# Kernel tuning notes

Measured on AMD Instinct MI355X. Metric: run time of the kernel, lower is better.

## Reference

```python
import jax, jax.numpy as jnp
import numpy as np

B, T, C, N = 4, 2048, 1024, 16
D = C // N


def setup_inputs() -> dict:
    key = jax.random.key(0)
    ks = jax.random.split(key, 10)
    s = 1.0 / np.sqrt(C)
    x = jax.random.normal(ks[0], (B, T, C), dtype=jnp.float32)
    token_mask = jax.random.randint(ks[1], (B, T), 0, 2, dtype=jnp.int32)
    token_mask = token_mask.at[:, 0].set(1)  # keep col 0 valid so no all--inf row
    inp = {"x": x, "token_mask": token_mask}
    for i, name in enumerate(["q", "k", "v", "p"]):
        inp[f"w{name}"] = jax.random.uniform(ks[2 + 2 * i], (C, C), jnp.float32, -s, s)
        inp[f"b{name}"] = jax.random.uniform(ks[3 + 2 * i], (C,), jnp.float32, -s, s)
    return inp


def reference(x, token_mask, wq, bq, wk, bk, wv, bv, wp, bp):
    # projections: nn.Linear computes x @ W.T + b
    q = (x @ wq.T + bq).reshape(B, T, N, D)
    k = (x @ wk.T + bk).reshape(B, T, N, D)
    v = (x @ wv.T + bv).reshape(B, T, N, D)
    # scores: (B, N, T, T)
    scores = jnp.einsum("bqnd,bknd->bnqk", q, k) / jnp.sqrt(jnp.float32(D))
    causal = jnp.tril(jnp.ones((T, T), dtype=bool))
    valid = causal[None, None] & (token_mask[:, None, None, :] != 0)
    scores = jnp.where(valid, scores, -jnp.inf)
    probs = jax.nn.softmax(scores, axis=-1)
    attn = jnp.einsum("bnqk,bknd->bqnd", probs, v).reshape(B, T, C)
    out = attn @ wp.T + bp
    return out
```

## Files before the change

kernel.cpp:

```cpp
#include <hip/hip_runtime.h>
#include <hip/hip_bf16.h>
#include <math.h>

typedef short bf16x8 __attribute__((ext_vector_type(8)));
typedef float f32x4 __attribute__((ext_vector_type(4)));

#if __has_builtin(__builtin_amdgcn_exp2f)
#define EXP2F(x) __builtin_amdgcn_exp2f(x)
#else
#define EXP2F(x) __expf(0.69314718056f * (x))
#endif

__device__ __forceinline__ unsigned short f2bf(float f) {
    union { float f; unsigned u; } v; v.f = f;
    unsigned r = v.u + 0x7fffu + ((v.u >> 16) & 1u);
    return (unsigned short)(r >> 16);
}

__device__ __forceinline__ unsigned pack_bf2(float a, float b) {
    __hip_bfloat162 h = __float22bfloat162_rn(float2{a, b});
    union { __hip_bfloat162 h; unsigned u; } c; c.h = h;
    return c.u;
}

__device__ __forceinline__ void gld_lds16(const unsigned short* g, const unsigned short* l) {
    __builtin_amdgcn_global_load_lds(
        (const __attribute__((address_space(1))) void*)g,
        (__attribute__((address_space(3))) void*)l, 16, 0, 0);
}

__global__ void cvt_f32_bf16(const float* __restrict__ src, unsigned short* __restrict__ dst, int n) {
    int i = (blockIdx.x * blockDim.x + threadIdx.x) * 4;
    if (i < n) {
        float4 f = *(const float4*)(src + i);
        ushort4 o;
        o.x = f2bf(f.x); o.y = f2bf(f.y); o.z = f2bf(f.z); o.w = f2bf(f.w);
        *(ushort4*)(dst + i) = o;
    }
}

__global__ void cvt4_f32_bf16(const float* s0, const float* s1, const float* s2, const float* s3,
                              unsigned short* d0, unsigned short* d1, unsigned short* d2,
                              unsigned short* d3, int n) {
    const float* s; unsigned short* d;
    switch (blockIdx.y) {
        case 0: s = s0; d = d0; break;
        case 1: s = s1; d = d1; break;
        case 2: s = s2; d = d2; break;
        default: s = s3; d = d3; break;
    }
    int i = (blockIdx.x * blockDim.x + threadIdx.x) * 4;
    if (i < n) {
        float4 f = *(const float4*)(s + i);
        ushort4 o;
        o.x = f2bf(f.x); o.y = f2bf(f.y); o.z = f2bf(f.z); o.w = f2bf(f.w);
        *(ushort4*)(d + i) = o;
    }
}

__global__ void mask_to_f(const int* __restrict__ tm, float* __restrict__ ma, int n) {
    int i = blockIdx.x * blockDim.x + threadIdx.x;
    if (i < n) ma[i] = tm[i] ? -24.0f : -__builtin_inff();
}

__global__ __launch_bounds__(256, 4) void gemm_bt(
        const unsigned short* __restrict__ A, const unsigned short* __restrict__ W,
        const float* __restrict__ b0p, const float* __restrict__ b1p,
        const float* __restrict__ b2p, float* __restrict__ outF,
        unsigned short* __restrict__ outB, unsigned short* __restrict__ vt,
        int M, int Nlog, int K) {
    __shared__ __align__(16) unsigned short As[2][128][32];
    __shared__ __align__(16) unsigned short Ws[2][128][32];
    const size_t BUFS = (size_t)8192 * 1024;
    const int m0 = blockIdx.y * 128, n0 = blockIdx.x * 128;
    const int tid = threadIdx.x, lane = tid & 63, w = tid >> 6;
    const int quad = lane >> 4, lc = lane & 15;
    const int wr = (w >> 1) * 64, wc = (w & 1) * 64;
    const int sr = lane >> 2;
    const int sc = (((lane & 3) ^ ((lane >> 3) & 3))) * 8;
    const int rp = (quad ^ ((lc >> 1) & 3)) * 8;

    const int buf = n0 >> 10;
    const float* bias = buf == 0 ? b0p : (buf == 1 ? b1p : b2p);

    auto stage = [&](int s, int k0) {
        gld_lds16(A + (size_t)(m0 + w * 32 +      sr) * K + k0 + sc, &As[s][w * 32     ][0]);
        gld_lds16(A + (size_t)(m0 + w * 32 + 16 + sr) * K + k0 + sc, &As[s][w * 32 + 16][0]);
        gld_lds16(W + (size_t)(n0 + w * 32 +      sr) * K + k0 + sc, &Ws[s][w * 32     ][0]);
        gld_lds16(W + (size_t)(n0 + w * 32 + 16 + sr) * K + k0 + sc, &Ws[s][w * 32 + 16][0]);
    };

    f32x4 acc[4][4] = {};
    stage(0, 0);

    for (int k0 = 0; k0 < K; k0 += 32) {
        const int cur = (k0 >> 5) & 1;
        __syncthreads();
        if (k0 + 32 < K) stage(cur ^ 1, k0 + 32);
        bf16x8 af[4], bw[4];
        #pragma unroll
        for (int i = 0; i < 4; ++i) af[i] = *(const bf16x8*)&As[cur][wr + i * 16 + lc][rp];
        #pragma unroll
        for (int j = 0; j < 4; ++j) bw[j] = *(const bf16x8*)&Ws[cur][wc + j * 16 + lc][rp];
        #pragma unroll
        for (int i = 0; i < 4; ++i)
            #pragma unroll
            for (int j = 0; j < 4; ++j)
                acc[i][j] = __builtin_amdgcn_mfma_f32_16x16x32_bf16(af[i], bw[j], acc[i][j], 0, 0, 0);
    }

    #pragma unroll
    for (int j = 0; j < 4; ++j) {
        int col = n0 + wc + j * 16 + lc;
        int coll = col & 1023;
        float bj = bias[coll];
        #pragma unroll
        for (int i = 0; i < 4; ++i) {
            int rowb = m0 + wr + i * 16 + quad * 4;
            if (buf == 2) {
                int bb = rowb >> 11, t = rowb & 2047;
                int hh = coll >> 6, dd = coll & 63;
                ushort4 o4;
                o4.x = f2bf(acc[i][j][0] + bj);
                o4.y = f2bf(acc[i][j][1] + bj);
                o4.z = f2bf(acc[i][j][2] + bj);
                o4.w = f2bf(acc[i][j][3] + bj);
                *(ushort4*)(vt + ((size_t)(bb * 16 + hh) * 64 + dd) * 2048 + t) = o4;
            } else {
                #pragma unroll
                for (int r = 0; r < 4; ++r) {
                    float v = acc[i][j][r] + bj;
                    size_t idx = (size_t)buf * BUFS + (size_t)(rowb + r) * 1024 + coll;
                    if (outB) outB[idx] = f2bf(v);
                    else      outF[idx] = v;
                }
            }
        }
    }
}

__global__ __launch_bounds__(256, 4) void attn_kernel(
        const unsigned short* __restrict__ Q, const unsigned short* __restrict__ K,
        const unsigned short* __restrict__ Vt, const float* __restrict__ maskadd,
        unsigned short* __restrict__ O) {
    const int T = 2048, C = 1024;
    __shared__ __align__(16) unsigned short Kl[64][64];
    __shared__ __align__(16) unsigned short Vl[2][64][64];
    __shared__ __align__(16) unsigned short Pl[4][16][72];

    const int pair = blockIdx.x;
    const int bn = blockIdx.y;
    const int b = bn >> 4, h = bn & 15;
    const int tid = threadIdx.x, w = tid >> 6, lane = tid & 63;
    const int quad = lane >> 4, lc = lane & 15;
    const float NEG_INF = -__builtin_inff();
    const float CSC = 0.18033688011112042f;

    const unsigned short* Kbh = K + (size_t)b * T * C + h * 64;
    const unsigned short* Vbh = Vt + (size_t)(b * 16 + h) * 64 * 2048;

    const int lrow = lane >> 3;
    const int swz8 = ((lane & 7) ^ (lrow & 7)) * 8;
    const int kb0 = (quad ^ (lc & 7)) * 8;

    auto stageK = [&](int kt) {
        #pragma unroll
        for (int ch = 0; ch < 2; ++ch)
            gld_lds16(Kbh + (size_t)(kt * 64 + w * 16 + ch * 8 + lrow) * C + swz8,
                      &Kl[w * 16 + ch * 8][0]);
    };
    auto stageV = [&](int kt, int s) {
        #pragma unroll
        for (int ch = 0; ch < 2; ++ch)
            gld_lds16(Vbh + (size_t)(w * 16 + ch * 8 + lrow) * 2048 + kt * 64 + swz8,
                      &Vl[s][w * 16 + ch * 8][0]);
    };

    #pragma unroll 1
    for (int half = 0; half < 2; ++half) {
        const int qt = half ? (31 - pair) : pair;

        if (half) __syncthreads();
        stageK(0);
        stageV(0, 0);

        size_t qrow = (size_t)(b * T + qt * 64 + w * 16 + lc) * C + h * 64;
        bf16x8 qb0 = *(const bf16x8*)(Q + qrow + quad * 8);
        bf16x8 qb1 = *(const bf16x8*)(Q + qrow + 32 + quad * 8);

        f32x4 oaccT[4] = {};
        float lsum = 0.f;
        const int qg = qt * 64 + w * 16 + lc;

        #pragma unroll 1
        for (int kt = 0; kt <= qt; ++kt) {
            const int slot = kt & 1;
            __syncthreads();

            f32x4 mk[4];
            #pragma unroll
            for (int j = 0; j < 4; ++j)
                mk[j] = *(const f32x4*)(maskadd + b * T + kt * 64 + j * 16 + quad * 4);

            f32x4 sacc[4] = {};
            #pragma unroll
            for (int j = 0; j < 4; ++j) {
                bf16x8 ka0 = *(const bf16x8*)&Kl[j * 16 + lc][kb0];
                bf16x8 ka1 = *(const bf16x8*)&Kl[j * 16 + lc][kb0 ^ 32];
                sacc[j] = __builtin_amdgcn_mfma_f32_16x16x32_bf16(ka0, qb0, sacc[j], 0, 0, 0);
                sacc[j] = __builtin_amdgcn_mfma_f32_16x16x32_bf16(ka1, qb1, sacc[j], 0, 0, 0);
            }

            __syncthreads();
            if (kt < qt) {
                stageK(kt + 1);
                stageV(kt + 1, slot ^ 1);
            }

            float p[4][4];
            #pragma unroll
            for (int j = 0; j < 4; ++j) {
                #pragma unroll
                for (int r = 0; r < 4; ++r) {
                    float sv = fmaf(sacc[j][r], CSC, mk[j][r]);
                    if (kt == qt) {
                        int kg = kt * 64 + j * 16 + quad * 4 + r;
                        if (kg > qg) sv = NEG_INF;
                    }
                    float pv = EXP2F(sv);
                    p[j][r] = pv;
                    lsum += pv;
                }
            }

            #pragma unroll
            for (int j = 0; j < 4; ++j) {
                uint2 pk;
                pk.x = pack_bf2(p[j][0], p[j][1]);
                pk.y = pack_bf2(p[j][2], p[j][3]);
                *(uint2*)&Pl[w][lc][j * 16 + quad * 4] = pk;
            }
            bf16x8 pb0 = *(const bf16x8*)&Pl[w][lc][quad * 8];
            bf16x8 pb1 = *(const bf16x8*)&Pl[w][lc][32 + quad * 8];

            #pragma unroll
            for (int jd = 0; jd < 4; ++jd) {
                bf16x8 va0 = *(const bf16x8*)&Vl[slot][jd * 16 + lc][kb0];
                bf16x8 va1 = *(const bf16x8*)&Vl[slot][jd * 16 + lc][kb0 ^ 32];
                oaccT[jd] = __builtin_amdgcn_mfma_f32_16x16x32_bf16(va0, pb0, oaccT[jd], 0, 0, 0);
                oaccT[jd] = __builtin_amdgcn_mfma_f32_16x16x32_bf16(va1, pb1, oaccT[jd], 0, 0, 0);
            }
        }

        lsum += __shfl_xor(lsum, 16, 64);
        lsum += __shfl_xor(lsum, 32, 64);
        float inv = 1.0f / lsum;
        size_t orow = (size_t)(b * T + qt * 64 + w * 16 + lc) * C + h * 64;
        #pragma unroll
        for (int jd = 0; jd < 4; ++jd) {
            ushort4 o4;
            o4.x = f2bf(oaccT[jd][0] * inv);
            o4.y = f2bf(oaccT[jd][1] * inv);
            o4.z = f2bf(oaccT[jd][2] * inv);
            o4.w = f2bf(oaccT[jd][3] * inv);
            *(ushort4*)(O + orow + jd * 16 + quad * 4) = o4;
        }
    }
}

extern "C" void kernel_launch(void* const* d_in, const int* in_sizes, int n_in,
                              void* d_out, int out_size, void* d_ws, size_t ws_size,
                              hipStream_t stream) {
    const float* x  = (const float*)d_in[0];
    const int* tm   = (const int*)d_in[1];
    const float* wq = (const float*)d_in[2]; const float* bq = (const float*)d_in[3];
    const float* wk = (const float*)d_in[4]; const float* bk = (const float*)d_in[5];
    const float* wv = (const float*)d_in[6]; const float* bv = (const float*)d_in[7];
    const float* wp = (const float*)d_in[8]; const float* bp = (const float*)d_in[9];
    float* out = (float*)d_out;

    const int Bv = 4, Tv = 2048, Cv = 1024;
    const size_t MT = (size_t)Bv * Tv;
    const size_t XN = MT * Cv;
    const size_t WN = (size_t)Cv * Cv;

    unsigned short* xb  = (unsigned short*)d_ws;
    unsigned short* wqb = xb  + XN;
    unsigned short* wkb = wqb + WN;
    unsigned short* wvb = wkb + WN;
    unsigned short* wpb = wvb + WN;
    unsigned short* Qb  = wpb + WN;
    unsigned short* Kb  = Qb + XN;
    unsigned short* Vtb = Kb + XN;
    unsigned short* Ab  = xb;
    float* maskadd = (float*)d_out;

    cvt_f32_bf16<<<XN / 1024, 256, 0, stream>>>(x, xb, (int)XN);
    cvt4_f32_bf16<<<dim3(WN / 1024, 4), 256, 0, stream>>>(wq, wk, wv, wp, wqb, wkb, wvb, wpb, (int)WN);
    mask_to_f<<<(int)(MT / 256), 256, 0, stream>>>(tm, maskadd, (int)MT);

    gemm_bt<<<dim3(24, 64), 256, 0, stream>>>(xb, wqb, bq, bk, bv, nullptr, Qb, Vtb, (int)MT, 3072, Cv);

    attn_kernel<<<dim3(16, Bv * 16), 256, 0, stream>>>(Qb, Kb, Vtb, maskadd, Ab);

    gemm_bt<<<dim3(8, 64), 256, 0, stream>>>(Ab, wpb, bp, bp, bp, out, nullptr, nullptr, (int)MT, 1024, Cv);
}
```

Before: 305.5 us.

## Widen attention blocks to 128 query rows and load GEMM W fragments directly

The attention kernel now uses 512-thread blocks covering 128 query rows, so each K/V tile staged in LDS is shared by eight waves instead of four. K and V staging is split across the two wave groups, and blocks are remapped on a flattened grid so each XCD handles a contiguous set of heads. The causal mask test moves into a separate diagonal-tile branch. Separately, the projection GEMM drops the LDS staging of W and has each lane read its W fragments straight from global memory, which lowers LDS use but adds uncoalesced global loads on every K step.

```diff
diff --git a/kernel.cpp b/kernel.cpp
--- a/kernel.cpp
+++ b/kernel.cpp
@@ -70,7 +70,6 @@
         unsigned short* __restrict__ outB, unsigned short* __restrict__ vt,
         int M, int Nlog, int K) {
     __shared__ __align__(16) unsigned short As[2][128][32];
-    __shared__ __align__(16) unsigned short Ws[2][128][32];
     const size_t BUFS = (size_t)8192 * 1024;
     const int m0 = blockIdx.y * 128, n0 = blockIdx.x * 128;
     const int tid = threadIdx.x, lane = tid & 63, w = tid >> 6;
@@ -83,25 +82,31 @@
     const int buf = n0 >> 10;
     const float* bias = buf == 0 ? b0p : (buf == 1 ? b1p : b2p);
 
-    auto stage = [&](int s, int k0) {
+    auto stageA = [&](int s, int k0) {
         gld_lds16(A + (size_t)(m0 + w * 32 +      sr) * K + k0 + sc, &As[s][w * 32     ][0]);
         gld_lds16(A + (size_t)(m0 + w * 32 + 16 + sr) * K + k0 + sc, &As[s][w * 32 + 16][0]);
-        gld_lds16(W + (size_t)(n0 + w * 32 +      sr) * K + k0 + sc, &Ws[s][w * 32     ][0]);
-        gld_lds16(W + (size_t)(n0 + w * 32 + 16 + sr) * K + k0 + sc, &Ws[s][w * 32 + 16][0]);
     };
 
+    const unsigned short* wp0 = W + (size_t)(n0 + wc +  0 + lc) * K + quad * 8;
+    const unsigned short* wp1 = W + (size_t)(n0 + wc + 16 + lc) * K + quad * 8;
+    const unsigned short* wp2 = W + (size_t)(n0 + wc + 32 + lc) * K + quad * 8;
+    const unsigned short* wp3 = W + (size_t)(n0 + wc + 48 + lc) * K + quad * 8;
+
     f32x4 acc[4][4] = {};
-    stage(0, 0);
+    stageA(0, 0);
 
     for (int k0 = 0; k0 < K; k0 += 32) {
         const int cur = (k0 >> 5) & 1;
         __syncthreads();
-        if (k0 + 32 < K) stage(cur ^ 1, k0 + 32);
-        bf16x8 af[4], bw[4];
+        if (k0 + 32 < K) stageA(cur ^ 1, k0 + 32);
+        bf16x8 bw[4];
+        bw[0] = *(const bf16x8*)(wp0 + k0);
+        bw[1] = *(const bf16x8*)(wp1 + k0);
+        bw[2] = *(const bf16x8*)(wp2 + k0);
+        bw[3] = *(const bf16x8*)(wp3 + k0);
+        bf16x8 af[4];
         #pragma unroll
         for (int i = 0; i < 4; ++i) af[i] = *(const bf16x8*)&As[cur][wr + i * 16 + lc][rp];
-        #pragma unroll
-        for (int j = 0; j < 4; ++j) bw[j] = *(const bf16x8*)&Ws[cur][wc + j * 16 + lc][rp];
         #pragma unroll
         for (int i = 0; i < 4; ++i)
             #pragma unroll
@@ -139,20 +144,23 @@
     }
 }
 
-__global__ __launch_bounds__(256, 4) void attn_kernel(
+__global__ __launch_bounds__(512, 4) void attn_kernel(
         const unsigned short* __restrict__ Q, const unsigned short* __restrict__ K,
         const unsigned short* __restrict__ Vt, const float* __restrict__ maskadd,
         unsigned short* __restrict__ O) {
     const int T = 2048, C = 1024;
     __shared__ __align__(16) unsigned short Kl[64][64];
     __shared__ __align__(16) unsigned short Vl[2][64][64];
-    __shared__ __align__(16) unsigned short Pl[4][16][72];
-
-    const int pair = blockIdx.x;
-    const int bn = blockIdx.y;
+    __shared__ __align__(16) unsigned short Pl[8][16][72];
+
+    const int bi = blockIdx.x;
+    const int xcd = bi & 7, rr = bi >> 3;
+    const int bn = xcd * 8 + (rr & 7);
+    const int pair = rr >> 3;
     const int b = bn >> 4, h = bn & 15;
     const int tid = threadIdx.x, w = tid >> 6, lane = tid & 63;
     const int quad = lane >> 4, lc = lane & 15;
+    const int wsub = w & 3, qhalf = w >> 2;
     const float NEG_INF = -__builtin_inff();
     const float CSC = 0.18033688011112042f;
 
@@ -163,38 +171,41 @@
     const int swz8 = ((lane & 7) ^ (lrow & 7)) * 8;
     const int kb0 = (quad ^ (lc & 7)) * 8;
 
-    auto stageK = [&](int kt) {
-        #pragma unroll
-        for (int ch = 0; ch < 2; ++ch)
-            gld_lds16(Kbh + (size_t)(kt * 64 + w * 16 + ch * 8 + lrow) * C + swz8,
-                      &Kl[w * 16 + ch * 8][0]);
+    auto stageKV = [&](int kt, int s) {
+        if (w < 4) {
+            #pragma unroll
+            for (int ch = 0; ch < 2; ++ch)
+                gld_lds16(Kbh + (size_t)(kt * 64 + w * 16 + ch * 8 + lrow) * C + swz8,
+                          &Kl[w * 16 + ch * 8][0]);
+        } else {
+            int wv = w - 4;
+            #pragma unroll
+            for (int ch = 0; ch < 2; ++ch)
+                gld_lds16(Vbh + (size_t)(wv * 16 + ch * 8 + lrow) * 2048 + kt * 64 + swz8,
+                          &Vl[s][wv * 16 + ch * 8][0]);
+        }
     };
-    auto stageV = [&](int kt, int s) {
-        #pragma unroll
-        for (int ch = 0; ch < 2; ++ch)
-            gld_lds16(Vbh + (size_t)(w * 16 + ch * 8 + lrow) * 2048 + kt * 64 + swz8,
-                      &Vl[s][w * 16 + ch * 8][0]);
-    };
 
     #pragma unroll 1
-    for (int half = 0; half < 2; ++half) {
-        const int qt = half ? (31 - pair) : pair;
-
-        if (half) __syncthreads();
-        stageK(0);
-        stageV(0, 0);
-
-        size_t qrow = (size_t)(b * T + qt * 64 + w * 16 + lc) * C + h * 64;
+    for (int hf = 0; hf < 2; ++hf) {
+        const int qt = hf ? (15 - pair) : pair;
+        const int kmax = 2 * qt + 1;
+
+        if (hf) __syncthreads();
+        stageKV(0, 0);
+
+        size_t qrow = (size_t)(b * T + qt * 128 + qhalf * 64 + wsub * 16 + lc) * C + h * 64;
         bf16x8 qb0 = *(const bf16x8*)(Q + qrow + quad * 8);
         bf16x8 qb1 = *(const bf16x8*)(Q + qrow + 32 + quad * 8);
 
         f32x4 oaccT[4] = {};
         float lsum = 0.f;
-        const int qg = qt * 64 + w * 16 + lc;
+        const int qg = qt * 128 + qhalf * 64 + wsub * 16 + lc;
 
         #pragma unroll 1
-        for (int kt = 0; kt <= qt; ++kt) {
+        for (int kt = 0; kt <= kmax; ++kt) {
             const int slot = kt & 1;
+            const bool dtile = (kt >= 2 * qt);
             __syncthreads();
 
             f32x4 mk[4];
@@ -212,25 +223,30 @@
             }
 
             __syncthreads();
-            if (kt < qt) {
-                stageK(kt + 1);
-                stageV(kt + 1, slot ^ 1);
-            }
+            if (kt < kmax) stageKV(kt + 1, slot ^ 1);
 
             float p[4][4];
-            #pragma unroll
-            for (int j = 0; j < 4; ++j) {
+            if (dtile) {
                 #pragma unroll
-                for (int r = 0; r < 4; ++r) {
-                    float sv = fmaf(sacc[j][r], CSC, mk[j][r]);
-                    if (kt == qt) {
+                for (int j = 0; j < 4; ++j)
+                    #pragma unroll
+                    for (int r = 0; r < 4; ++r) {
+                        float sv = fmaf(sacc[j][r], CSC, mk[j][r]);
                         int kg = kt * 64 + j * 16 + quad * 4 + r;
                         if (kg > qg) sv = NEG_INF;
+                        float pv = EXP2F(sv);
+                        p[j][r] = pv;
+                        lsum += pv;
                     }
-                    float pv = EXP2F(sv);
-                    p[j][r] = pv;
-                    lsum += pv;
-                }
+            } else {
+                #pragma unroll
+                for (int j = 0; j < 4; ++j)
+                    #pragma unroll
+                    for (int r = 0; r < 4; ++r) {
+                        float pv = EXP2F(fmaf(sacc[j][r], CSC, mk[j][r]));
+                        p[j][r] = pv;
+                        lsum += pv;
+                    }
             }
 
             #pragma unroll
@@ -255,7 +271,7 @@
         lsum += __shfl_xor(lsum, 16, 64);
         lsum += __shfl_xor(lsum, 32, 64);
         float inv = 1.0f / lsum;
-        size_t orow = (size_t)(b * T + qt * 64 + w * 16 + lc) * C + h * 64;
+        size_t orow = qrow;
         #pragma unroll
         for (int jd = 0; jd < 4; ++jd) {
             ushort4 o4;
@@ -301,7 +317,7 @@
 
     gemm_bt<<<dim3(24, 64), 256, 0, stream>>>(xb, wqb, bq, bk, bv, nullptr, Qb, Vtb, (int)MT, 3072, Cv);
 
-    attn_kernel<<<dim3(16, Bv * 16), 256, 0, stream>>>(Qb, Kb, Vtb, maskadd, Ab);
+    attn_kernel<<<dim3(512), 512, 0, stream>>>(Qb, Kb, Vtb, maskadd, Ab);
 
     gemm_bt<<<dim3(8, 64), 256, 0, stream>>>(Ab, wpb, bp, bp, bp, out, nullptr, nullptr, (int)MT, 1024, Cv);
 }
```

After: 338.2 us. 10.7% more time.
